# Kernel tuning notes

Measured on AMD Instinct MI355X. Metric: run time of the kernel, lower is better.

Reference implementation:

```python
import jax, jax.numpy as jnp
import numpy as np

_EPS = 1e-5
_NORM_EPS = 1e-6


def setup_inputs() -> dict:
    key = jax.random.key(0)
    k1, k2 = jax.random.split(key)
    B, S, D_IN, D_OUT = 4, 8192, 2048, 2048
    x = jax.random.normal(k1, (B, S, D_IN), dtype=jnp.float32)
    gamma = jnp.ones((D_IN,), dtype=jnp.float32)  # RMSNorm scale
    # kaiming_uniform-like init: bound = sqrt(6/((1+5)*fan_in)) = 1/sqrt(fan_in)
    bound = 1.0 / np.sqrt(D_IN)
    W = jax.random.uniform(k2, (D_OUT, D_IN), dtype=jnp.float32, minval=-bound, maxval=bound)
    return {"x": x, "gamma": gamma, "W": W}


def reference(x, gamma, W):
    # RMSNorm (pre-norm baked into BitLinear)
    rms = jax.lax.rsqrt(jnp.mean(x * x, axis=-1, keepdims=True) + _NORM_EPS)
    xn = x * rms * gamma

    # Per-token absmax int8 activation fake-quant with STE
    a_scale = 127.0 / (jnp.max(jnp.abs(xn), axis=-1, keepdims=True) + _EPS)
    x_q = jnp.clip(jnp.round(xn * a_scale), -128.0, 127.0) / a_scale
    x_ste = xn + jax.lax.stop_gradient(x_q - xn)

    # Per-tensor ternary weight fake-quant (absmean scale) with STE
    w_scale = 1.0 / (jnp.mean(jnp.abs(W)) + _EPS)
    w_q = jnp.clip(jnp.round(W * w_scale), -1.0, 1.0) / w_scale
    w_ste = W + jax.lax.stop_gradient(w_q - W)

    # Linear: [B,S,Din] x [Dout,Din]^T -> [B,S,Dout]
    return jnp.einsum('bsd,od->bso', x_ste, w_ste)
```

## Files before the change

kernel.cpp:

```cpp
#include <hip/hip_runtime.h>
#include <stdint.h>

#define K_DIM 2048
#define N_DIM 2048
#define M_TOK 32768

typedef float v4f __attribute__((ext_vector_type(4)));
typedef int   v4i __attribute__((ext_vector_type(4)));

#define WS_PART   0
#define WS_STAT   8192
#define WS_TSCALE 8448
#define WS_WT     262144
#define WS_QX     4456448

__device__ __forceinline__ void gload_lds16(const void* g, void* l) {
    __builtin_amdgcn_global_load_lds(
        (const __attribute__((address_space(1))) unsigned int*)g,
        (__attribute__((address_space(3))) unsigned int*)l,
        16, 0, 0);
}

__device__ __forceinline__ unsigned int pack4(int a, int b, int c, int d) {
    return (unsigned int)(a & 255) | ((unsigned int)(b & 255) << 8) |
           ((unsigned int)(c & 255) << 16) | ((unsigned int)(d & 255) << 24);
}

__global__ __launch_bounds__(256) void wabs_partial(const float* __restrict__ W,
                                                    double* __restrict__ part) {
    const int t = threadIdx.x, b = blockIdx.x;
    const float* p = W + (size_t)b * 4096;
    double s = 0.0;
#pragma unroll
    for (int i = 0; i < 4; ++i) {
        float4 v = *(const float4*)(p + i * 1024 + t * 4);
        s += (double)fabsf(v.x) + (double)fabsf(v.y) +
             (double)fabsf(v.z) + (double)fabsf(v.w);
    }
    int lane = t & 63, wv = t >> 6;
#pragma unroll
    for (int off = 32; off > 0; off >>= 1) s += __shfl_down(s, off, 64);
    __shared__ double red[4];
    if (lane == 0) red[wv] = s;
    __syncthreads();
    if (t == 0) part[b] = red[0] + red[1] + red[2] + red[3];
}

__global__ __launch_bounds__(256) void wfinal(const double* __restrict__ part,
                                              float* __restrict__ wstat) {
    const int t = threadIdx.x;
    double s = part[t] + part[t + 256] + part[t + 512] + part[t + 768];
    int lane = t & 63, wv = t >> 6;
#pragma unroll
    for (int off = 32; off > 0; off >>= 1) s += __shfl_down(s, off, 64);
    __shared__ double red[4];
    if (lane == 0) red[wv] = s;
    __syncthreads();
    if (t == 0) {
        double mean = (red[0] + red[1] + red[2] + red[3]) * (1.0 / 4194304.0);
        float winv = (float)mean + 1e-5f;
        wstat[0] = winv;
        wstat[1] = 1.0f / winv;
    }
}

__global__ __launch_bounds__(256) void wquant(const float* __restrict__ W,
                                              const float* __restrict__ wstat,
                                              int8_t* __restrict__ wt) {
    const float wsc = wstat[1];
    size_t i = ((size_t)blockIdx.x * 256 + threadIdx.x) * 4;
    float4 v = *(const float4*)(W + i);
    int q0 = (int)rintf(fminf(fmaxf(v.x * wsc, -1.0f), 1.0f));
    int q1 = (int)rintf(fminf(fmaxf(v.y * wsc, -1.0f), 1.0f));
    int q2 = (int)rintf(fminf(fmaxf(v.z * wsc, -1.0f), 1.0f));
    int q3 = (int)rintf(fminf(fmaxf(v.w * wsc, -1.0f), 1.0f));
    *(unsigned int*)(wt + i) = pack4(q0, q1, q2, q3);
}

__global__ __launch_bounds__(256) void rmsnorm_quant(const float* __restrict__ x,
                                                     const float* __restrict__ gamma,
                                                     const float* __restrict__ wstat,
                                                     int8_t* __restrict__ qx,
                                                     float* __restrict__ tscale) {
    const int row = blockIdx.x;
    const int t = threadIdx.x;
    const float* xr = x + (size_t)row * K_DIM;

    float4 v0 = *(const float4*)(xr + t * 4);
    float4 v1 = *(const float4*)(xr + 1024 + t * 4);
    float4 g0 = *(const float4*)(gamma + t * 4);
    float4 g1 = *(const float4*)(gamma + 1024 + t * 4);

    float ss = v0.x * v0.x + v0.y * v0.y + v0.z * v0.z + v0.w * v0.w +
               v1.x * v1.x + v1.y * v1.y + v1.z * v1.z + v1.w * v1.w;

    __shared__ float red[8];
    {
        int lane = t & 63, wv = t >> 6;
#pragma unroll
        for (int off = 32; off > 0; off >>= 1) ss += __shfl_down(ss, off, 64);
        if (lane == 0) red[wv] = ss;
        __syncthreads();
        ss = red[0] + red[1] + red[2] + red[3];
    }
    const float rms = 1.0f / sqrtf(ss * (1.0f / 2048.0f) + 1e-6f);

    float xn[8];
    xn[0] = v0.x * rms * g0.x;  xn[1] = v0.y * rms * g0.y;
    xn[2] = v0.z * rms * g0.z;  xn[3] = v0.w * rms * g0.w;
    xn[4] = v1.x * rms * g1.x;  xn[5] = v1.y * rms * g1.y;
    xn[6] = v1.z * rms * g1.z;  xn[7] = v1.w * rms * g1.w;

    float am = 0.0f;
#pragma unroll
    for (int j = 0; j < 8; ++j) am = fmaxf(am, fabsf(xn[j]));
    {
        int lane = t & 63, wv = t >> 6;
#pragma unroll
        for (int off = 32; off > 0; off >>= 1) am = fmaxf(am, __shfl_down(am, off, 64));
        if (lane == 0) red[4 + wv] = am;
        __syncthreads();
        am = fmaxf(fmaxf(red[4], red[5]), fmaxf(red[6], red[7]));
    }
    const float amp = am + 1e-5f;
    const float ascale = 127.0f / amp;

    int q[8];
#pragma unroll
    for (int j = 0; j < 8; ++j)
        q[j] = (int)rintf(fminf(fmaxf(xn[j] * ascale, -128.0f), 127.0f));

    int8_t* qr = qx + (size_t)row * K_DIM;
    *(unsigned int*)(qr + t * 4)        = pack4(q[0], q[1], q[2], q[3]);
    *(unsigned int*)(qr + 1024 + t * 4) = pack4(q[4], q[5], q[6], q[7]);

    if (t == 0) tscale[row] = amp * wstat[0] * (1.0f / 127.0f);
}

__global__ __launch_bounds__(256) void gemm_i8(const int8_t* __restrict__ qx,
                                               const int8_t* __restrict__ wt,
                                               const float* __restrict__ tscale,
                                               float* __restrict__ out) {
    __shared__ int8_t lds_a[128 * 128];
    __shared__ int8_t lds_b[128 * 128];

    const int t = threadIdx.x;
    const int lane = t & 63;
    const int wv = t >> 6;
    const int bn0 = blockIdx.x * 128;
    const int bm0 = blockIdx.y * 128;
    const int wm = (wv >> 1) * 64;
    const int wn = (wv & 1) * 64;
    const int quad = lane >> 4;
    const int l16 = lane & 15;

    v4i acc[4][4];
    const v4i izero = {0, 0, 0, 0};
#pragma unroll
    for (int i = 0; i < 4; ++i)
#pragma unroll
        for (int j = 0; j < 4; ++j) acc[i][j] = izero;

    int srow[4], sjg[4];
#pragma unroll
    for (int cc = 0; cc < 4; ++cc) {
        int c = cc * 256 + t;
        srow[cc] = c >> 3;
        sjg[cc] = (c & 7) ^ (srow[cc] & 7);
    }
    const size_t baseA = (size_t)bm0 * K_DIM;
    const size_t baseB = (size_t)bn0 * K_DIM;

    for (int k0 = 0; k0 < K_DIM; k0 += 128) {
        __syncthreads();
#pragma unroll
        for (int cc = 0; cc < 4; ++cc) {
            const int8_t* ga = qx + baseA + (size_t)srow[cc] * K_DIM + k0 + sjg[cc] * 16;
            const int8_t* gb = wt + baseB + (size_t)srow[cc] * K_DIM + k0 + sjg[cc] * 16;
            int8_t* la = lds_a + (cc * 256 + wv * 64) * 16;
            int8_t* lb = lds_b + (cc * 256 + wv * 64) * 16;
            gload_lds16(ga, la);
            gload_lds16(gb, lb);
        }
        __syncthreads();

#pragma unroll
        for (int kh = 0; kh < 2; ++kh) {
            v4i af[4], bfr[4];
            const int j = kh * 4 + quad;
#pragma unroll
            for (int ti = 0; ti < 4; ++ti) {
                const int ra = wm + ti * 16 + l16;
                af[ti] = *(const v4i*)(lds_a + ra * 128 + ((j ^ (ra & 7)) * 16));
                const int rb = wn + ti * 16 + l16;
                bfr[ti] = *(const v4i*)(lds_b + rb * 128 + ((j ^ (rb & 7)) * 16));
            }
#pragma unroll
            for (int ti = 0; ti < 4; ++ti)
#pragma unroll
                for (int tj = 0; tj < 4; ++tj)
                    acc[ti][tj] = __builtin_amdgcn_mfma_i32_16x16x64_i8(
                        af[ti], bfr[tj], acc[ti][tj], 0, 0, 0);
        }
    }

#pragma unroll
    for (int ti = 0; ti < 4; ++ti) {
#pragma unroll
        for (int r = 0; r < 4; ++r) {
            const int row = bm0 + wm + ti * 16 + quad * 4 + r;
            const float s = tscale[row];
            float* op = out + (size_t)row * N_DIM + bn0 + wn + l16;
#pragma unroll
            for (int tj = 0; tj < 4; ++tj)
                op[tj * 16] = (float)acc[ti][tj][r] * s;
        }
    }
}

extern "C" void kernel_launch(void* const* d_in, const int* in_sizes, int n_in,
                              void* d_out, int out_size, void* d_ws, size_t ws_size,
                              hipStream_t stream) {
    const float* x     = (const float*)d_in[0];
    const float* gamma = (const float*)d_in[1];
    const float* W     = (const float*)d_in[2];
    float* out = (float*)d_out;

    char* ws = (char*)d_ws;
    double* wpart  = (double*)(ws + WS_PART);
    float*  wstat  = (float*)(ws + WS_STAT);
    float*  tscale = (float*)(ws + WS_TSCALE);
    int8_t* wt     = (int8_t*)(ws + WS_WT);
    int8_t* qx     = (int8_t*)(ws + WS_QX);

    wabs_partial<<<1024, 256, 0, stream>>>(W, wpart);
    wfinal<<<1, 256, 0, stream>>>(wpart, wstat);
    wquant<<<4096, 256, 0, stream>>>(W, wstat, wt);
    rmsnorm_quant<<<M_TOK, 256, 0, stream>>>(x, gamma, wstat, qx, tscale);

    dim3 grid(N_DIM / 128, M_TOK / 128);
    gemm_i8<<<grid, 256, 0, stream>>>(qx, wt, tscale, out);
}
```

Baseline: 641.7 us.

## Rewrite int8 GEMM with 256x256 tiles, double-buffered LDS pipeline and block swizzle

The int8 MFMA GEMM moves from a 128x128 tile with 256 threads and single-buffered LDS to a 256x256 tile with 512 threads (8 waves, 128x64 per wave). LDS is double-buffered, and async global-to-LDS loads for the next K tile are interleaved with MFMA phases using vmcnt waits, barriers and setprio. A block-index swizzle groups blocks for better L2 reuse. This aims to hide memory latency and raise arithmetic intensity, at the cost of higher register use (128 accumulator VGPRs) and 128KB of LDS per block, which lowers occupancy.

Result: faster. 595.5 us (-7.2%).

```diff
diff --git a/kernel.cpp b/kernel.cpp
--- a/kernel.cpp
+++ b/kernel.cpp
@@ -137,85 +137,153 @@
     if (t == 0) tscale[row] = amp * wstat[0] * (1.0f / 127.0f);
 }
 
-__global__ __launch_bounds__(256) void gemm_i8(const int8_t* __restrict__ qx,
-                                               const int8_t* __restrict__ wt,
-                                               const float* __restrict__ tscale,
-                                               float* __restrict__ out) {
-    __shared__ int8_t lds_a[128 * 128];
-    __shared__ int8_t lds_b[128 * 128];
+
+__device__ __forceinline__ v4i ldsfrag(const int8_t* p, int row, int j0) {
+    return *(const v4i*)(p + row * 128 + (((j0) ^ (row & 7)) << 4));
+}
+
+template <int Q, bool LOADB>
+__device__ __forceinline__ void ph_load(const int8_t* pA, const int8_t* pB,
+                                        v4i (&af)[2][2], v4i (&bf)[4][2],
+                                        int wm, int wn, int l16, int quad) {
+    if constexpr (LOADB) {
+#pragma unroll
+        for (int nt = 0; nt < 4; ++nt)
+#pragma unroll
+            for (int ks = 0; ks < 2; ++ks)
+                bf[nt][ks] = ldsfrag(pB, wn + nt * 16 + l16, ks * 4 + quad);
+    }
+#pragma unroll
+    for (int mt = 0; mt < 2; ++mt)
+#pragma unroll
+        for (int ks = 0; ks < 2; ++ks)
+            af[mt][ks] = ldsfrag(pA, wm + (2 * Q + mt) * 16 + l16, ks * 4 + quad);
+}
+
+template <int Q>
+__device__ __forceinline__ void ph_mma(v4i (&acc)[8][4], const v4i (&af)[2][2],
+                                       const v4i (&bf)[4][2]) {
+#pragma unroll
+    for (int mt = 0; mt < 2; ++mt)
+#pragma unroll
+        for (int nt = 0; nt < 4; ++nt)
+#pragma unroll
+            for (int ks = 0; ks < 2; ++ks)
+                acc[2 * Q + mt][nt] = __builtin_amdgcn_mfma_i32_16x16x64_i8(
+                    af[mt][ks], bf[nt][ks], acc[2 * Q + mt][nt], 0, 0, 0);
+}
+
+#define VMC(n) asm volatile("s_waitcnt vmcnt(" #n ")" ::: "memory")
+
+__global__ __launch_bounds__(512, 2) void gemm_i8(const int8_t* __restrict__ qx,
+                                                  const int8_t* __restrict__ wt,
+                                                  const float* __restrict__ tscale,
+                                                  float* __restrict__ out) {
+    __shared__ int8_t ldsA[2][32768];
+    __shared__ int8_t ldsB[2][32768];
 
     const int t = threadIdx.x;
     const int lane = t & 63;
-    const int wv = t >> 6;
-    const int bn0 = blockIdx.x * 128;
-    const int bm0 = blockIdx.y * 128;
-    const int wm = (wv >> 1) * 64;
-    const int wn = (wv & 1) * 64;
+    const int w = t >> 6;
+    const int l16 = lane & 15;
     const int quad = lane >> 4;
-    const int l16 = lane & 15;
-
-    v4i acc[4][4];
-    const v4i izero = {0, 0, 0, 0};
-#pragma unroll
-    for (int i = 0; i < 4; ++i)
-#pragma unroll
-        for (int j = 0; j < 4; ++j) acc[i][j] = izero;
-
-    int srow[4], sjg[4];
-#pragma unroll
-    for (int cc = 0; cc < 4; ++cc) {
-        int c = cc * 256 + t;
-        srow[cc] = c >> 3;
-        sjg[cc] = (c & 7) ^ (srow[cc] & 7);
-    }
+
+    const int bid = blockIdx.x;
+    const int swz = (bid & 7) * 128 + (bid >> 3);
+    const int bn0 = (swz & 7) * 256;
+    const int bm0 = (swz >> 3) * 256;
+
+    const int wm = (w >> 2) * 128;
+    const int wn = (w & 3) * 64;
+
+    const int srow = t >> 3;
+    const int sjx  = ((t & 7) ^ (srow & 7)) << 4;
+    const int wbase = w * 1024;
     const size_t baseA = (size_t)bm0 * K_DIM;
     const size_t baseB = (size_t)bn0 * K_DIM;
 
-    for (int k0 = 0; k0 < K_DIM; k0 += 128) {
-        __syncthreads();
-#pragma unroll
-        for (int cc = 0; cc < 4; ++cc) {
-            const int8_t* ga = qx + baseA + (size_t)srow[cc] * K_DIM + k0 + sjg[cc] * 16;
-            const int8_t* gb = wt + baseB + (size_t)srow[cc] * K_DIM + k0 + sjg[cc] * 16;
-            int8_t* la = lds_a + (cc * 256 + wv * 64) * 16;
-            int8_t* lb = lds_b + (cc * 256 + wv * 64) * 16;
-            gload_lds16(ga, la);
-            gload_lds16(gb, lb);
-        }
-        __syncthreads();
-
-#pragma unroll
-        for (int kh = 0; kh < 2; ++kh) {
-            v4i af[4], bfr[4];
-            const int j = kh * 4 + quad;
-#pragma unroll
-            for (int ti = 0; ti < 4; ++ti) {
-                const int ra = wm + ti * 16 + l16;
-                af[ti] = *(const v4i*)(lds_a + ra * 128 + ((j ^ (ra & 7)) * 16));
-                const int rb = wn + ti * 16 + l16;
-                bfr[ti] = *(const v4i*)(lds_b + rb * 128 + ((j ^ (rb & 7)) * 16));
-            }
-#pragma unroll
-            for (int ti = 0; ti < 4; ++ti)
-#pragma unroll
-                for (int tj = 0; tj < 4; ++tj)
-                    acc[ti][tj] = __builtin_amdgcn_mfma_i32_16x16x64_i8(
-                        af[ti], bfr[tj], acc[ti][tj], 0, 0, 0);
-        }
-    }
-
-#pragma unroll
-    for (int ti = 0; ti < 4; ++ti) {
+#define STAGE_A(buf, h, kt) do {                                                   \
+        const int8_t* _s = qx + baseA + (size_t)((h) * 128 + srow) * K_DIM +       \
+                           (kt) * 128 + sjx;                                       \
+        gload_lds16(_s,              &ldsA[buf][(h) * 16384 + wbase]);             \
+        gload_lds16(_s + 64 * K_DIM, &ldsA[buf][(h) * 16384 + 8192 + wbase]);      \
+    } while (0)
+#define STAGE_B(buf, h, kt) do {                                                   \
+        const int8_t* _s = wt + baseB + (size_t)((h) * 128 + srow) * K_DIM +       \
+                           (kt) * 128 + sjx;                                       \
+        gload_lds16(_s,              &ldsB[buf][(h) * 16384 + wbase]);             \
+        gload_lds16(_s + 64 * K_DIM, &ldsB[buf][(h) * 16384 + 8192 + wbase]);      \
+    } while (0)
+
+    v4i acc[8][4];
+    const v4i izero = {0, 0, 0, 0};
+#pragma unroll
+    for (int i = 0; i < 8; ++i)
+#pragma unroll
+        for (int j = 0; j < 4; ++j) acc[i][j] = izero;
+
+    v4i bf[4][2];
+    const int8_t* pA0 = ldsA[0];
+    const int8_t* pA1 = ldsA[1];
+    const int8_t* pB0 = ldsB[0];
+    const int8_t* pB1 = ldsB[1];
+
+    STAGE_B(0, 0, 0);
+    STAGE_B(0, 1, 0);
+    STAGE_A(0, 0, 0);
+    STAGE_A(0, 1, 0);
+    STAGE_B(1, 0, 1);
+    STAGE_B(1, 1, 1);
+    VMC(4);
+    __builtin_amdgcn_s_barrier();
+
+#define DO_PHASE(Q, LOADB, PA, PB, STAGE_STMT, TAIL_STMT)           \
+    {                                                               \
+        v4i af[2][2];                                               \
+        ph_load<Q, LOADB>(PA, PB, af, bf, wm, wn, l16, quad);       \
+        STAGE_STMT;                                                 \
+        __builtin_amdgcn_s_barrier();                               \
+        asm volatile("s_waitcnt lgkmcnt(0)" ::: "memory");          \
+        __builtin_amdgcn_sched_barrier(0);                          \
+        __builtin_amdgcn_s_setprio(1);                              \
+        ph_mma<Q>(acc, af, bf);                                     \
+        __builtin_amdgcn_s_setprio(0);                              \
+        TAIL_STMT;                                                  \
+        __builtin_amdgcn_s_barrier();                               \
+    }
+
+#pragma unroll 1
+    for (int i = 0; i < 8; ++i) {
+        const int kt1 = 2 * i + 1;
+        const int kt2 = 2 * i + 2;
+        const int kt3 = 2 * i + 3;
+        const bool pf = (i < 7);
+        DO_PHASE(0, true,  pA0, pB0, STAGE_A(1, 0, kt1), (void)0);
+        DO_PHASE(1, false, pA0, pB0, STAGE_A(1, 1, kt1), (void)0);
+        DO_PHASE(2, false, pA0, pB0, if (pf) STAGE_B(0, 0, kt2), (void)0);
+        DO_PHASE(3, false, pA0, pB0, if (pf) STAGE_B(0, 1, kt2),
+                 if (pf) { VMC(4); } else { VMC(0); });
+        DO_PHASE(0, true,  pA1, pB1, if (pf) STAGE_A(0, 0, kt2), (void)0);
+        DO_PHASE(1, false, pA1, pB1, if (pf) STAGE_A(0, 1, kt2), (void)0);
+        DO_PHASE(2, false, pA1, pB1, if (pf) STAGE_B(1, 0, kt3), (void)0);
+        DO_PHASE(3, false, pA1, pB1, if (pf) STAGE_B(1, 1, kt3), VMC(4));
+    }
+
+#pragma unroll
+    for (int mt = 0; mt < 8; ++mt) {
 #pragma unroll
         for (int r = 0; r < 4; ++r) {
-            const int row = bm0 + wm + ti * 16 + quad * 4 + r;
+            const int row = bm0 + wm + mt * 16 + quad * 4 + r;
             const float s = tscale[row];
             float* op = out + (size_t)row * N_DIM + bn0 + wn + l16;
 #pragma unroll
-            for (int tj = 0; tj < 4; ++tj)
-                op[tj * 16] = (float)acc[ti][tj][r] * s;
+            for (int nt = 0; nt < 4; ++nt)
+                op[nt * 16] = (float)acc[mt][nt][r] * s;
         }
     }
+#undef DO_PHASE
+#undef STAGE_A
+#undef STAGE_B
 }
 
 extern "C" void kernel_launch(void* const* d_in, const int* in_sizes, int n_in,
@@ -238,6 +306,5 @@
     wquant<<<4096, 256, 0, stream>>>(W, wstat, wt);
     rmsnorm_quant<<<M_TOK, 256, 0, stream>>>(x, gamma, wstat, qx, tscale);
 
-    dim3 grid(N_DIM / 128, M_TOK / 128);
-    gemm_i8<<<grid, 256, 0, stream>>>(qx, wt, tscale, out);
-}
+    gemm_i8<<<dim3(1024), dim3(512), 0, stream>>>(qx, wt, tscale, out);
+}
```
